# Kernel tuning notes

Hardware: AMD Instinct MI355X
Metric: run time of the kernel (lower is better)

Reference implementation:

```python
import jax, jax.numpy as jnp
import numpy as np
import math

H = W = 256
TILE = 64
HT, WT = H // TILE, W // TILE
NT = HT * WT
TAN_FOV = 0.5                      # tan(FoV/2) for both axes
FOCAL = W / (2.0 * TAN_FOV)        # 256.0
RADII_MULT = 5.0                   # kwargs.get('radii_multiplier', 5)
N_GAUSS = 1024


def setup_inputs() -> dict:
    key = jax.random.key(0)
    k1, k2, k3, k4, k5 = jax.random.split(key, 5)
    # Gaussians inside the view frustum so tiles receive splats
    z = jax.random.uniform(k1, (N_GAUSS,), minval=1.5, maxval=8.0)
    xy = (jax.random.uniform(k2, (N_GAUSS, 2)) - 0.5) * (2.0 * TAN_FOV * 0.9) * z[:, None]
    means3d = jnp.concatenate([xy, z[:, None]], axis=-1).astype(jnp.float32)
    opacity = jax.random.uniform(k3, (N_GAUSS, 1), minval=0.05, maxval=0.95, dtype=jnp.float32)
    scale3d = jax.random.uniform(k4, (N_GAUSS,), minval=0.01, maxval=0.06, dtype=jnp.float32)
    features = jax.random.uniform(k5, (N_GAUSS, 3), dtype=jnp.float32)
    viewmatrix = jnp.eye(4, dtype=jnp.float32)
    # perspective projection, row-vector convention (points @ P)
    znear, zfar = 0.01, 100.0
    P = np.zeros((4, 4), np.float32)
    P[0, 0] = 1.0 / TAN_FOV
    P[1, 1] = 1.0 / TAN_FOV
    P[2, 2] = zfar / (zfar - znear)
    P[2, 3] = -(zfar * znear) / (zfar - znear)
    P[3, 2] = 1.0
    projmatrix = jnp.asarray(P.T)
    return {"means3d": means3d, "opacity": opacity, "scale3d": scale3d,
            "features": features, "viewmatrix": viewmatrix, "projmatrix": projmatrix}


def _tile_pix():
    # pix_coord[y, x] = (x, y), split into NT tiles of TILE*TILE pixels
    pix = jnp.stack(jnp.meshgrid(jnp.arange(W), jnp.arange(H), indexing='xy'), axis=-1).astype(jnp.float32)
    tiles = pix.reshape(HT, TILE, WT, TILE, 2).transpose(0, 2, 1, 3, 4).reshape(NT, TILE * TILE, 2)
    v_idx, u_idx = jnp.meshgrid(jnp.arange(HT), jnp.arange(WT), indexing='ij')
    u0 = (u_idx.reshape(-1) * TILE).astype(jnp.float32)
    v0 = (v_idx.reshape(-1) * TILE).astype(jnp.float32)
    return tiles, u0, v0


def reference(means3d, opacity, scale3d, features, viewmatrix, projmatrix):
    # --- projection_ndc ---
    points_o = jnp.concatenate([means3d, jnp.ones_like(means3d[..., :1])], axis=-1)   # [N,4]
    points_h = points_o @ viewmatrix @ projmatrix
    p_proj = points_h / (points_h[..., -1:] + 1e-6)
    p_view = points_o @ viewmatrix
    depths = p_view[:, 2]
    # --- build_scale_2d (tx/ty computed in torch but unused; only tz matters) ---
    t = means3d @ viewmatrix[:3, :3] + viewmatrix[3:4, :3]
    tz = t[..., 2]
    scale2d = jnp.stack([scale3d * FOCAL / tz, scale3d * FOCAL / tz], axis=-1)        # [N,2]
    means2d = jnp.stack([((p_proj[..., 0] + 1) * W - 1.0) * 0.5,
                         ((p_proj[..., 1] + 1) * H - 1.0) * 0.5], axis=-1)            # [N,2]
    # --- rects ---
    radii = jnp.max(scale2d, axis=-1) * RADII_MULT
    rect_min = jnp.stack([jnp.clip(means2d[:, 0] - radii, 0.0, W - 1.0),
                          jnp.clip(means2d[:, 1] - radii, 0.0, H - 1.0)], axis=-1)
    rect_max = jnp.stack([jnp.clip(means2d[:, 0] + radii, 0.0, W - 1.0),
                          jnp.clip(means2d[:, 1] + radii, 0.0, H - 1.0)], axis=-1)
    # --- global front-to-back depth sort; per-tile masking with alpha=0 is
    #     mathematically identical to the torch per-tile filter+sort composite ---
    order = jnp.argsort(depths)
    m2, op, col = means2d[order], opacity[order], features[order]
    dep = depths[order]
    s2sq = jnp.max(scale2d[order], axis=-1) ** 2
    rmin, rmax = rect_min[order], rect_max[order]
    tiles, u0s, v0s = _tile_pix()

    def render_tile(tile_pix, u0, v0):
        tlx = jnp.maximum(rmin[:, 0], u0)
        tly = jnp.maximum(rmin[:, 1], v0)
        brx = jnp.minimum(rmax[:, 0], u0 + TILE - 1.0)
        bry = jnp.minimum(rmax[:, 1], v0 + TILE - 1.0)
        mask = (brx > tlx) & (bry > tly)                                              # [N]
        dx2 = ((tile_pix[:, None, 0] - m2[None, :, 0]) ** 2 +
               (tile_pix[:, None, 1] - m2[None, :, 1]) ** 2)                          # [P,N]
        gw = jnp.exp(-0.5 * dx2 / s2sq[None])                                         # isotropic RKHS weight
        alpha = jnp.minimum(gw[..., None] * op[None], 0.99) * mask[None, :, None]     # [P,N,1]
        T = jnp.cumprod(jnp.concatenate([jnp.ones_like(alpha[:, :1]), 1.0 - alpha[:, :-1]], axis=1), axis=1)
        w = alpha * T
        acc = w.sum(axis=1)                                                           # [P,1]
        c = jnp.clip((w * col[None]).sum(axis=1) + (1.0 - acc), 0.0, 1.0)             # white bkgd
        d = (w * dep[None, :, None]).sum(axis=1)
        return c, d, acc

    cols, deps_t, accs = jax.vmap(render_tile)(tiles, u0s, v0s)

    def untile(x):
        return x.reshape(HT, WT, TILE, TILE, -1).transpose(0, 2, 1, 3, 4).reshape(H, W, -1)

    return untile(cols), untile(deps_t), untile(accs)
```

## Files before the change

kernel.cpp:

```cpp
#include <hip/hip_runtime.h>
#include <math.h>

#define NG 1024
#define HH 256
#define WW 256
#define TILE_PX 64
#define WT 4
#define FOCAL_F 256.0f
#define RADII_MULT_F 5.0f
#define SEG 256


__global__ __launch_bounds__(256) void prep_rank_kernel(
    const float* __restrict__ means3d, const float* __restrict__ opacity,
    const float* __restrict__ scale3d, const float* __restrict__ features,
    const float* __restrict__ viewm, const float* __restrict__ projm,
    float* __restrict__ ws)
{
    __shared__ float s_dep[NG];
    __shared__ int s_rank[64][4];

    const int t = threadIdx.x;
    const int l = t & 63;
    const int q = t >> 6;
    const int gid = blockIdx.x * 64 + l;

    const float v2 = viewm[2], v6 = viewm[6], v10 = viewm[10], v14 = viewm[14];
#pragma unroll
    for (int c = 0; c < NG / 256; c++) {
        const int g = c * 256 + t;
        const float mx = means3d[g * 3 + 0];
        const float my = means3d[g * 3 + 1];
        const float mz = means3d[g * 3 + 2];
        s_dep[g] = mx * v2 + my * v6 + mz * v10 + v14;
    }
    __syncthreads();

    const float myd = s_dep[gid];
    const float4* s4 = (const float4*)s_dep;
    int rank = 0;
#pragma unroll 8
    for (int j4 = q * (NG / 16); j4 < (q + 1) * (NG / 16); j4++) {
        const float4 d = s4[j4];
        const int j = j4 * 4;
        rank += (d.x < myd || (d.x == myd && j + 0 < gid)) ? 1 : 0;
        rank += (d.y < myd || (d.y == myd && j + 1 < gid)) ? 1 : 0;
        rank += (d.z < myd || (d.z == myd && j + 2 < gid)) ? 1 : 0;
        rank += (d.w < myd || (d.w == myd && j + 3 < gid)) ? 1 : 0;
    }
    s_rank[l][q] = rank;
    __syncthreads();

    if (t < 64) {
        rank = s_rank[l][0] + s_rank[l][1] + s_rank[l][2] + s_rank[l][3];

        float V[16], P[16];
#pragma unroll
        for (int j = 0; j < 16; j++) { V[j] = viewm[j]; P[j] = projm[j]; }

        const float mx = means3d[gid * 3 + 0];
        const float my = means3d[gid * 3 + 1];
        const float mz = means3d[gid * 3 + 2];

        const float q0 = mx * V[0] + my * V[4] + mz * V[8]  + V[12];
        const float q1 = mx * V[1] + my * V[5] + mz * V[9]  + V[13];
        const float q2 = mx * V[2] + my * V[6] + mz * V[10] + V[14];
        const float q3 = mx * V[3] + my * V[7] + mz * V[11] + V[15];
        const float h0 = q0 * P[0] + q1 * P[4] + q2 * P[8]  + q3 * P[12];
        const float h1 = q0 * P[1] + q1 * P[5] + q2 * P[9]  + q3 * P[13];
        const float h3 = q0 * P[3] + q1 * P[7] + q2 * P[11] + q3 * P[15];

        const float inv_w = 1.0f / (h3 + 1e-6f);
        const float m2x = ((h0 * inv_w + 1.0f) * (float)WW - 1.0f) * 0.5f;
        const float m2y = ((h1 * inv_w + 1.0f) * (float)HH - 1.0f) * 0.5f;

        const float s2 = scale3d[gid] * FOCAL_F / q2;
        const float radii = s2 * RADII_MULT_F;
        const float kexp = -0.72134752044448170f / (s2 * s2);

        const float rminx = fminf(fmaxf(m2x - radii, 0.0f), (float)(WW - 1));
        const float rminy = fminf(fmaxf(m2y - radii, 0.0f), (float)(HH - 1));
        const float rmaxx = fminf(fmaxf(m2x + radii, 0.0f), (float)(WW - 1));
        const float rmaxy = fminf(fmaxf(m2y + radii, 0.0f), (float)(HH - 1));

        float4* wsv = (float4*)ws;
        wsv[rank]          = make_float4(rminx, rmaxx, rminy, rmaxy);
        wsv[NG + rank]     = make_float4(m2x, m2y, kexp, opacity[gid]);
        wsv[2 * NG + rank] = make_float4(features[gid * 3 + 0],
                                         features[gid * 3 + 1],
                                         features[gid * 3 + 2], q2);
    }
}

__global__ __launch_bounds__(256) void render_kernel(
    const float* __restrict__ ws, float* __restrict__ out)
{
    __shared__ float4 s_list[4 * SEG][2];
    __shared__ int s_cnt[4];

    const int blk  = blockIdx.x;
    const int tile = blk >> 4;
    const int rg   = blk & 15;
    const int u0 = (tile & (WT - 1)) * TILE_PX;
    const int v0 = (tile / WT) * TILE_PX;
    const int t = threadIdx.x;
    const int l = t & 63;
    const int w = t >> 6;

    const int pxi = u0 + l;
    const int pyi = v0 + rg * 4 + w;
    const float px = (float)pxi;
    const float py = (float)pyi;
    const float u0f  = (float)u0;
    const float u1f  = (float)(u0 + TILE_PX - 1);
    const float py0f = (float)(v0 + rg * 4);
    const float py3f = py0f + 3.0f;

    const float4* rect4 = (const float4*)ws;
    const float4* attrA = rect4 + NG;
    const float4* attrB = rect4 + 2 * NG;

    int cnt = 0;
#pragma unroll
    for (int it = 0; it < 4; it++) {
        const int g = (w << 8) + (it << 6) + l;
        const float4 rc = rect4[g];
        const bool pass = (fminf(rc.y, u1f) > fmaxf(rc.x, u0f)) &&
                          (rc.z <= py3f) && (rc.w >= py0f);
        const unsigned long long m = __ballot(pass);
        if (pass) {
            const int off = (w << 8) + cnt + __popcll(m & ((1ull << l) - 1ull));
            s_list[off][0] = attrA[g];
            s_list[off][1] = attrB[g];
        }
        cnt += __popcll(m);
    }
    if (l == 0) s_cnt[w] = cnt;
    __syncthreads();

    float T = 1.0f, cr = 0.0f, cg = 0.0f, cb = 0.0f, dsum = 0.0f, accsum = 0.0f;
    for (int s = 0; s < 4; s++) {
        const int n = s_cnt[s];
        const int base = s << 8;
        for (int e = 0; e < n; e++) {
            const float4 a = s_list[base + e][0];
            const float4 b = s_list[base + e][1];
            const float dx = px - a.x;
            const float dy = py - a.y;
            const float d2 = fmaf(dx, dx, dy * dy);
            const float gw = exp2f(d2 * a.z);
            const float alpha = fminf(gw * a.w, 0.99f);
            const float wgt = alpha * T;
            cr   = fmaf(wgt, b.x, cr);
            cg   = fmaf(wgt, b.y, cg);
            cb   = fmaf(wgt, b.z, cb);
            dsum = fmaf(wgt, b.w, dsum);
            accsum += wgt;
            T = fmaf(-alpha, T, T);
        }
    }

    const float bg = 1.0f - accsum;
    cr = fminf(fmaxf(cr + bg, 0.0f), 1.0f);
    cg = fminf(fmaxf(cg + bg, 0.0f), 1.0f);
    cb = fminf(fmaxf(cb + bg, 0.0f), 1.0f);

    const int pix = pyi * WW + pxi;
    out[pix * 3 + 0] = cr;
    out[pix * 3 + 1] = cg;
    out[pix * 3 + 2] = cb;
    out[WW * HH * 3 + pix] = dsum;
    out[WW * HH * 4 + pix] = accsum;
}

extern "C" void kernel_launch(void* const* d_in, const int* in_sizes, int n_in,
                              void* d_out, int out_size, void* d_ws, size_t ws_size,
                              hipStream_t stream) {
    const float* means3d  = (const float*)d_in[0];
    const float* opacity  = (const float*)d_in[1];
    const float* scale3d  = (const float*)d_in[2];
    const float* features = (const float*)d_in[3];
    const float* viewm    = (const float*)d_in[4];
    const float* projm    = (const float*)d_in[5];
    float* ws  = (float*)d_ws;
    float* out = (float*)d_out;

    prep_rank_kernel<<<16, 256, 0, stream>>>(means3d, opacity, scale3d, features,
                                             viewm, projm, ws);
    render_kernel<<<256, 256, 0, stream>>>(ws, out);
}
```

Before: 77.77 us.

## Fuse projection, culling and per-block depth sort into the render kernel

Result: faster. 69.63 us (-10.5%).

```diff
diff --git a/kernel.cpp b/kernel.cpp
--- a/kernel.cpp
+++ b/kernel.cpp
@@ -8,94 +8,15 @@
 #define WT 4
 #define FOCAL_F 256.0f
 #define RADII_MULT_F 5.0f
-#define SEG 256
 
-
-__global__ __launch_bounds__(256) void prep_rank_kernel(
+__global__ __launch_bounds__(256) void fused_render_kernel(
     const float* __restrict__ means3d, const float* __restrict__ opacity,
     const float* __restrict__ scale3d, const float* __restrict__ features,
     const float* __restrict__ viewm, const float* __restrict__ projm,
-    float* __restrict__ ws)
+    float* __restrict__ out)
 {
-    __shared__ float s_dep[NG];
-    __shared__ int s_rank[64][4];
-
-    const int t = threadIdx.x;
-    const int l = t & 63;
-    const int q = t >> 6;
-    const int gid = blockIdx.x * 64 + l;
-
-    const float v2 = viewm[2], v6 = viewm[6], v10 = viewm[10], v14 = viewm[14];
-#pragma unroll
-    for (int c = 0; c < NG / 256; c++) {
-        const int g = c * 256 + t;
-        const float mx = means3d[g * 3 + 0];
-        const float my = means3d[g * 3 + 1];
-        const float mz = means3d[g * 3 + 2];
-        s_dep[g] = mx * v2 + my * v6 + mz * v10 + v14;
-    }
-    __syncthreads();
-
-    const float myd = s_dep[gid];
-    const float4* s4 = (const float4*)s_dep;
-    int rank = 0;
-#pragma unroll 8
-    for (int j4 = q * (NG / 16); j4 < (q + 1) * (NG / 16); j4++) {
-        const float4 d = s4[j4];
-        const int j = j4 * 4;
-        rank += (d.x < myd || (d.x == myd && j + 0 < gid)) ? 1 : 0;
-        rank += (d.y < myd || (d.y == myd && j + 1 < gid)) ? 1 : 0;
-        rank += (d.z < myd || (d.z == myd && j + 2 < gid)) ? 1 : 0;
-        rank += (d.w < myd || (d.w == myd && j + 3 < gid)) ? 1 : 0;
-    }
-    s_rank[l][q] = rank;
-    __syncthreads();
-
-    if (t < 64) {
-        rank = s_rank[l][0] + s_rank[l][1] + s_rank[l][2] + s_rank[l][3];
-
-        float V[16], P[16];
-#pragma unroll
-        for (int j = 0; j < 16; j++) { V[j] = viewm[j]; P[j] = projm[j]; }
-
-        const float mx = means3d[gid * 3 + 0];
-        const float my = means3d[gid * 3 + 1];
-        const float mz = means3d[gid * 3 + 2];
-
-        const float q0 = mx * V[0] + my * V[4] + mz * V[8]  + V[12];
-        const float q1 = mx * V[1] + my * V[5] + mz * V[9]  + V[13];
-        const float q2 = mx * V[2] + my * V[6] + mz * V[10] + V[14];
-        const float q3 = mx * V[3] + my * V[7] + mz * V[11] + V[15];
-        const float h0 = q0 * P[0] + q1 * P[4] + q2 * P[8]  + q3 * P[12];
-        const float h1 = q0 * P[1] + q1 * P[5] + q2 * P[9]  + q3 * P[13];
-        const float h3 = q0 * P[3] + q1 * P[7] + q2 * P[11] + q3 * P[15];
-
-        const float inv_w = 1.0f / (h3 + 1e-6f);
-        const float m2x = ((h0 * inv_w + 1.0f) * (float)WW - 1.0f) * 0.5f;
-        const float m2y = ((h1 * inv_w + 1.0f) * (float)HH - 1.0f) * 0.5f;
-
-        const float s2 = scale3d[gid] * FOCAL_F / q2;
-        const float radii = s2 * RADII_MULT_F;
-        const float kexp = -0.72134752044448170f / (s2 * s2);
-
-        const float rminx = fminf(fmaxf(m2x - radii, 0.0f), (float)(WW - 1));
-        const float rminy = fminf(fmaxf(m2y - radii, 0.0f), (float)(HH - 1));
-        const float rmaxx = fminf(fmaxf(m2x + radii, 0.0f), (float)(WW - 1));
-        const float rmaxy = fminf(fmaxf(m2y + radii, 0.0f), (float)(HH - 1));
-
-        float4* wsv = (float4*)ws;
-        wsv[rank]          = make_float4(rminx, rmaxx, rminy, rmaxy);
-        wsv[NG + rank]     = make_float4(m2x, m2y, kexp, opacity[gid]);
-        wsv[2 * NG + rank] = make_float4(features[gid * 3 + 0],
-                                         features[gid * 3 + 1],
-                                         features[gid * 3 + 2], q2);
-    }
-}
-
-__global__ __launch_bounds__(256) void render_kernel(
-    const float* __restrict__ ws, float* __restrict__ out)
-{
-    __shared__ float4 s_list[4 * SEG][2];
+    __shared__ float4 s_sorted[NG][2];
+    __shared__ unsigned long long s_key[NG];
     __shared__ int s_cnt[4];
 
     const int blk  = blockIdx.x;
@@ -116,48 +37,112 @@
     const float py0f = (float)(v0 + rg * 4);
     const float py3f = py0f + 3.0f;
 
-    const float4* rect4 = (const float4*)ws;
-    const float4* attrA = rect4 + NG;
-    const float4* attrB = rect4 + 2 * NG;
+    float V[16], P[16];
+#pragma unroll
+    for (int j = 0; j < 16; j++) { V[j] = viewm[j]; P[j] = projm[j]; }
 
+    float mx[4], my[4], mz[4], sc[4], op[4], fr[4], fg[4], fb[4];
+#pragma unroll
+    for (int k = 0; k < 4; k++) {
+        const int g = (k << 8) + t;
+        mx[k] = means3d[g * 3 + 0];
+        my[k] = means3d[g * 3 + 1];
+        mz[k] = means3d[g * 3 + 2];
+        sc[k] = scale3d[g];
+        op[k] = opacity[g];
+        fr[k] = features[g * 3 + 0];
+        fg[k] = features[g * 3 + 1];
+        fb[k] = features[g * 3 + 2];
+    }
+
+    float4 eA[4], eB[4];
+    unsigned long long ekey[4];
+    int epos[4];
     int cnt = 0;
 #pragma unroll
-    for (int it = 0; it < 4; it++) {
-        const int g = (w << 8) + (it << 6) + l;
-        const float4 rc = rect4[g];
-        const bool pass = (fminf(rc.y, u1f) > fmaxf(rc.x, u0f)) &&
-                          (rc.z <= py3f) && (rc.w >= py0f);
+    for (int k = 0; k < 4; k++) {
+        const int g = (k << 8) + t;
+        const float q0 = mx[k] * V[0] + my[k] * V[4] + mz[k] * V[8]  + V[12];
+        const float q1 = mx[k] * V[1] + my[k] * V[5] + mz[k] * V[9]  + V[13];
+        const float q2 = mx[k] * V[2] + my[k] * V[6] + mz[k] * V[10] + V[14];
+        const float q3 = mx[k] * V[3] + my[k] * V[7] + mz[k] * V[11] + V[15];
+        const float h0 = q0 * P[0] + q1 * P[4] + q2 * P[8]  + q3 * P[12];
+        const float h1 = q0 * P[1] + q1 * P[5] + q2 * P[9]  + q3 * P[13];
+        const float h3 = q0 * P[3] + q1 * P[7] + q2 * P[11] + q3 * P[15];
+
+        const float inv_w = 1.0f / (h3 + 1e-6f);
+        const float m2x = ((h0 * inv_w + 1.0f) * (float)WW - 1.0f) * 0.5f;
+        const float m2y = ((h1 * inv_w + 1.0f) * (float)HH - 1.0f) * 0.5f;
+
+        const float s2 = sc[k] * FOCAL_F / q2;
+        const float radii = s2 * RADII_MULT_F;
+        const float kexp = -0.72134752044448170f / (s2 * s2);
+
+        const float rminx = fminf(fmaxf(m2x - radii, 0.0f), (float)(WW - 1));
+        const float rminy = fminf(fmaxf(m2y - radii, 0.0f), (float)(HH - 1));
+        const float rmaxx = fminf(fmaxf(m2x + radii, 0.0f), (float)(WW - 1));
+        const float rmaxy = fminf(fmaxf(m2y + radii, 0.0f), (float)(HH - 1));
+
+        const bool pass = (fminf(rmaxx, u1f) > fmaxf(rminx, u0f)) &&
+                          (rminy <= py3f) && (rmaxy >= py0f);
         const unsigned long long m = __ballot(pass);
+        epos[k] = -1;
         if (pass) {
             const int off = (w << 8) + cnt + __popcll(m & ((1ull << l) - 1ull));
-            s_list[off][0] = attrA[g];
-            s_list[off][1] = attrB[g];
+            epos[k] = off;
+            eA[k] = make_float4(m2x, m2y, kexp, op[k]);
+            eB[k] = make_float4(fr[k], fg[k], fb[k], q2);
+            unsigned int ub = __float_as_uint(q2);
+            ub = (ub & 0x80000000u) ? ~ub : (ub | 0x80000000u);
+            ekey[k] = ((unsigned long long)ub << 32) | (unsigned int)g;
+            s_key[off] = ekey[k];
         }
         cnt += __popcll(m);
     }
     if (l == 0) s_cnt[w] = cnt;
     __syncthreads();
 
+    const int c0 = s_cnt[0], c1 = s_cnt[1], c2 = s_cnt[2], c3 = s_cnt[3];
+    const int n = c0 + c1 + c2 + c3;
+
+    int rk[4] = {0, 0, 0, 0};
+#pragma unroll
+    for (int s = 0; s < 4; s++) {
+        const int cn = (s == 0) ? c0 : (s == 1) ? c1 : (s == 2) ? c2 : c3;
+        const int base = s << 8;
+        for (int j = 0; j < cn; j++) {
+            const unsigned long long k2 = s_key[base + j];
+#pragma unroll
+            for (int k = 0; k < 4; k++)
+                if (epos[k] >= 0 && k2 < ekey[k]) rk[k]++;
+        }
+    }
+
+#pragma unroll
+    for (int k = 0; k < 4; k++) {
+        if (epos[k] >= 0) {
+            s_sorted[rk[k]][0] = eA[k];
+            s_sorted[rk[k]][1] = eB[k];
+        }
+    }
+    __syncthreads();
+
     float T = 1.0f, cr = 0.0f, cg = 0.0f, cb = 0.0f, dsum = 0.0f, accsum = 0.0f;
-    for (int s = 0; s < 4; s++) {
-        const int n = s_cnt[s];
-        const int base = s << 8;
-        for (int e = 0; e < n; e++) {
-            const float4 a = s_list[base + e][0];
-            const float4 b = s_list[base + e][1];
-            const float dx = px - a.x;
-            const float dy = py - a.y;
-            const float d2 = fmaf(dx, dx, dy * dy);
-            const float gw = exp2f(d2 * a.z);
-            const float alpha = fminf(gw * a.w, 0.99f);
-            const float wgt = alpha * T;
-            cr   = fmaf(wgt, b.x, cr);
-            cg   = fmaf(wgt, b.y, cg);
-            cb   = fmaf(wgt, b.z, cb);
-            dsum = fmaf(wgt, b.w, dsum);
-            accsum += wgt;
-            T = fmaf(-alpha, T, T);
-        }
+    for (int e = 0; e < n; e++) {
+        const float4 a = s_sorted[e][0];
+        const float4 b = s_sorted[e][1];
+        const float dx = px - a.x;
+        const float dy = py - a.y;
+        const float d2 = fmaf(dx, dx, dy * dy);
+        const float gw = exp2f(d2 * a.z);
+        const float alpha = fminf(gw * a.w, 0.99f);
+        const float wgt = alpha * T;
+        cr   = fmaf(wgt, b.x, cr);
+        cg   = fmaf(wgt, b.y, cg);
+        cb   = fmaf(wgt, b.z, cb);
+        dsum = fmaf(wgt, b.w, dsum);
+        accsum += wgt;
+        T = fmaf(-alpha, T, T);
     }
 
     const float bg = 1.0f - accsum;
@@ -182,10 +167,8 @@
     const float* features = (const float*)d_in[3];
     const float* viewm    = (const float*)d_in[4];
     const float* projm    = (const float*)d_in[5];
-    float* ws  = (float*)d_ws;
     float* out = (float*)d_out;
 
-    prep_rank_kernel<<<16, 256, 0, stream>>>(means3d, opacity, scale3d, features,
-                                             viewm, projm, ws);
-    render_kernel<<<256, 256, 0, stream>>>(ws, out);
+    fused_render_kernel<<<256, 256, 0, stream>>>(means3d, opacity, scale3d,
+                                                 features, viewm, projm, out);
 }
```
